# Kernel tuning notes

Measured on AMD Instinct MI355X. Metric: run time of the kernel, lower is better.

The kernel has to match this reference:

```python
import jax, jax.numpy as jnp
import numpy as np

CODEBOOK_NUM = 8192
CODEBOOK_DIM = 256
BETA = 1.0


def setup_inputs() -> dict:
    key = jax.random.key(0)
    k1, k2 = jax.random.split(key)
    z = jax.random.normal(k1, (8, CODEBOOK_DIM, 16, 16, 16), dtype=jnp.float32)
    # torch init: uniform_(-1/codebook_num, 1/codebook_num)
    codebook = jax.random.uniform(
        k2, (CODEBOOK_NUM, CODEBOOK_DIM), dtype=jnp.float32,
        minval=-1.0 / CODEBOOK_NUM, maxval=1.0 / CODEBOOK_NUM)
    return {"z": z, "codebook": codebook}


def reference(z, codebook):
    # z: [B, C, D, H, W] -> [B, D, H, W, C]
    zp = jnp.transpose(z, (0, 2, 3, 4, 1))
    z_flat = zp.reshape(-1, codebook.shape[1])  # [N, C]
    # squared euclidean distances via ||a||^2 + ||b||^2 - 2 a.b
    d = (jnp.sum(z_flat ** 2, axis=1, keepdims=True)
         + jnp.sum(codebook ** 2, axis=1)
         - 2.0 * jnp.matmul(z_flat, codebook.T))  # [N, K]
    idx = jnp.argmin(d, axis=1)  # [N]
    z_q = codebook[idx].reshape(zp.shape)  # [B, D, H, W, C]
    sg = jax.lax.stop_gradient
    loss = jnp.mean((sg(z_q) - zp) ** 2) + BETA * jnp.mean((z_q - sg(zp)) ** 2)
    # straight-through estimator
    z_q_st = zp + sg(z_q - zp)
    out = jnp.transpose(z_q_st, (0, 4, 1, 2, 3))  # back to [B, C, D, H, W]
    return out, loss, idx
```

## Files before the change

### kernel.cpp

```cpp
#include <hip/hip_runtime.h>
#include <hip/hip_bf16.h>
#include <stdint.h>
#include <stddef.h>

typedef unsigned short ushort_t;
typedef unsigned int uint_t;

typedef __attribute__((ext_vector_type(8))) short short8;
typedef __attribute__((ext_vector_type(4))) float floatx4;
typedef __attribute__((ext_vector_type(16))) float floatx16;
typedef __attribute__((ext_vector_type(4))) uint_t uintx4;

#define N_ROWS 32768
#define K_ENT  8192
#define CDIM   256
#define OUT_ELEMS 8388608
#define LOSS_OFF  8388608
#define IDX_OFF   8388609
#define CAP_Q  44
#define MARGIN    2.0e-4f

__device__ __forceinline__ ushort_t f2bf(float f) {
    uint_t x = __float_as_uint(f);
    uint_t r = (x + 0x7fffu + ((x >> 16) & 1u)) >> 16;
    return (ushort_t)r;
}


__device__ __forceinline__ void gload_lds16(const ushort_t* g, ushort_t* s) {
    __builtin_amdgcn_global_load_lds(
        (__attribute__((address_space(1))) void*)(g),
        (__attribute__((address_space(3))) void*)(s), 16, 0, 0);
}

__global__ __launch_bounds__(256) void k_prep(const float* __restrict__ zin,
                                              const float* __restrict__ cb,
                                              ushort_t* __restrict__ zsw,
                                              ushort_t* __restrict__ cbsw,
                                              float* __restrict__ ztf,
                                              int* __restrict__ cnt,
                                              int* __restrict__ cnt2,
                                              double* __restrict__ acc) {
    int bid = blockIdx.x;
    if (bid >= 2048) {
        int t = (bid - 2048) * 256 + threadIdx.x;
        if (t < N_ROWS * 4) cnt[t] = 0;
        if (t == 0) { *acc = 0.0; *cnt2 = 0; }
        int ent = t >> 5;
        int c0  = (t & 31) << 3;
        const float* p = cb + (size_t)ent * CDIM + c0;
        floatx4 f0 = *(const floatx4*)p;
        floatx4 f1 = *(const floatx4*)(p + 4);
        uintx4 pk;
        pk[0] = (uint_t)f2bf(f0[0]) | ((uint_t)f2bf(f0[1]) << 16);
        pk[1] = (uint_t)f2bf(f0[2]) | ((uint_t)f2bf(f0[3]) << 16);
        pk[2] = (uint_t)f2bf(f1[0]) | ((uint_t)f2bf(f1[1]) << 16);
        pk[3] = (uint_t)f2bf(f1[2]) | ((uint_t)f2bf(f1[3]) << 16);
        int idx = (ent >> 5) * 8192 + (c0 >> 4) * 512 + ((c0 >> 3) & 1) * 256 + (ent & 31) * 8;
        *(uintx4*)(cbsw + idx) = pk;
        return;
    }
    __shared__ float lds[64][65];
    int c0 = (bid & 3) << 6;
    int s0 = ((bid >> 2) & 63) << 6;
    int b  = bid >> 8;
    int tid = threadIdx.x;
    int j = tid & 63, ib = tid >> 6;
    const float* zb = zin + ((size_t)b << 20);
#pragma unroll
    for (int rr = 0; rr < 16; ++rr) {
        int i = rr * 4 + ib;
        lds[i][j] = zb[(size_t)(c0 + i) * 4096 + s0 + j];
    }
    __syncthreads();
#pragma unroll
    for (int it = 0; it < 2; ++it) {
        int item = it * 256 + tid;
        int sl = item >> 3;
        int ch = item & 7;
        int row = (b << 12) + s0 + sl;
        int cg  = c0 + ch * 8;
        uintx4 pk;
        floatx4 f0, f1;
#pragma unroll
        for (int q = 0; q < 4; ++q) {
            float a = lds[ch * 8 + 2 * q][sl];
            float bqv = lds[ch * 8 + 2 * q + 1][sl];
            pk[q] = (uint_t)f2bf(a) | ((uint_t)f2bf(bqv) << 16);
        }
#pragma unroll
        for (int q = 0; q < 4; ++q) {
            f0[q] = lds[ch * 8 + q][sl];
            f1[q] = lds[ch * 8 + 4 + q][sl];
        }
        int idx = (row >> 5) * 8192 + (cg >> 4) * 512 + ((cg >> 3) & 1) * 256 + (row & 31) * 8;
        *(uintx4*)(zsw + idx) = pk;
        if (ztf) {
            *(floatx4*)(ztf + (size_t)row * 256 + cg) = f0;
            *(floatx4*)(ztf + (size_t)row * 256 + cg + 4) = f1;
        }
    }
}

__device__ __forceinline__ void screen_emit(const floatx16& acc, float& rmx,
                                            int& cur, int hi, int2* slist,
                                            int ent0) {
    float t0 = fmaxf(fmaxf(acc[0], acc[1]), fmaxf(acc[2], acc[3]));
    float t1 = fmaxf(fmaxf(acc[4], acc[5]), fmaxf(acc[6], acc[7]));
    float t2 = fmaxf(fmaxf(acc[8], acc[9]), fmaxf(acc[10], acc[11]));
    float t3 = fmaxf(fmaxf(acc[12], acc[13]), fmaxf(acc[14], acc[15]));
    float mxo = fmaxf(fmaxf(t0, t1), fmaxf(t2, t3));
    float mx = fmaxf(mxo, __shfl_xor(mxo, 32));
    float rm = fmaxf(rmx, mx);
    rmx = rm;
    float thr = rm - MARGIN;
    if (__any(mxo >= thr)) {
        uint_t mask = 0u;
#pragma unroll
        for (int r = 0; r < 16; ++r)
            if (acc[r] >= thr) mask |= (1u << r);
        int p  = __popc(mask);
        int pp = __shfl_xor(p, 32);
        int s  = cur + (hi ? pp : 0);
        cur += p + pp;
        if (mask) {
#pragma unroll
            for (int r = 0; r < 16; ++r) {
                if (mask & (1u << r)) {
                    if (s < CAP_Q)
                        slist[s] = make_int2(ent0 + (r & 3) + 8 * (r >> 2),
                                             __float_as_int(acc[r]));
                    ++s;
                }
            }
        }
    }
}

__global__ __launch_bounds__(256, 4) void k_screen(const ushort_t* __restrict__ zsw,
                                                   const ushort_t* __restrict__ cbsw,
                                                   int2* __restrict__ surv,
                                                   int* __restrict__ cnt) {
    __shared__ ushort_t bt[2][8192];
    int tid = threadIdx.x;
    int w = tid >> 6, l = tid & 63;
    int bid = blockIdx.x;
    int q  = bid & 3;
    int RB = (bid >> 2) * 128;
    int n = RB + w * 32 + (l & 31);
    int cidx = n * 4 + q;
    int2* slist = surv + (size_t)cidx * CAP_Q;
    int tile0 = q * 64;
    int hi = l & 32;

    auto stage = [&](int t, int b) {
        const ushort_t* gs = cbsw + (size_t)(tile0 + t) * 8192;
#pragma unroll
        for (int j = 0; j < 4; ++j)
            gload_lds16(gs + j * 2048 + tid * 8, &bt[b][j * 2048 + w * 512]);
    };

    stage(0, 0);

    short8 zfr[16];
    {
        const ushort_t* pz = zsw + (size_t)((RB >> 5) + w) * 8192 + l * 8;
#pragma unroll
        for (int s = 0; s < 16; ++s)
            zfr[s] = *(const short8*)(pz + s * 512);
    }
    __syncthreads();

    float rmx = -3.0e38f;
    int cur = 0;
    int esub = (l >> 5) * 4;

    floatx16 accA, accB;
    auto compute = [&](floatx16& acc, int b) {
        const ushort_t* bb = &bt[b][l * 8];
#pragma unroll
        for (int i = 0; i < 16; ++i) acc[i] = 0.f;
#pragma unroll
        for (int s = 0; s < 16; ++s) {
            short8 a = *(const short8*)(bb + s * 512);
            acc = __builtin_amdgcn_mfma_f32_32x32x16_bf16(a, zfr[s], acc, 0, 0, 0);
        }
    };
    auto ent_of = [&](int t) { return (tile0 + t) * 32 + esub; };

    stage(1, 1);
    __builtin_amdgcn_s_setprio(1);
    compute(accA, 0);
    __builtin_amdgcn_s_setprio(0);
    __syncthreads();

    for (int t = 1; t < 63; t += 2) {
        stage(t + 1, (t + 1) & 1);
        __builtin_amdgcn_s_setprio(1);
        compute(accB, t & 1);
        screen_emit(accA, rmx, cur, hi, slist, ent_of(t - 1));
        __builtin_amdgcn_s_setprio(0);
        __syncthreads();
        stage(t + 2, t & 1);
        __builtin_amdgcn_s_setprio(1);
        compute(accA, (t + 1) & 1);
        screen_emit(accB, rmx, cur, hi, slist, ent_of(t));
        __builtin_amdgcn_s_setprio(0);
        __syncthreads();
    }
    __builtin_amdgcn_s_setprio(1);
    compute(accB, 1);
    screen_emit(accA, rmx, cur, hi, slist, ent_of(62));
    __builtin_amdgcn_s_setprio(0);
    screen_emit(accB, rmx, cur, hi, slist, ent_of(63));

    if (!hi) cnt[cidx] = cur;
}

__global__ __launch_bounds__(256) void k_refine(const float* __restrict__ zin,
                                                const float* __restrict__ ztf,
                                                const float* __restrict__ cb,
                                                const int2* __restrict__ surv,
                                                const int* __restrict__ cnt,
                                                int* __restrict__ idxi,
                                                float* __restrict__ idxf) {
    __shared__ float zr[4][256];
    int w = threadIdx.x >> 6, l = threadIdx.x & 63;
    int n = blockIdx.x * 4 + w;
    if (ztf) {
        const float* zrow = ztf + (size_t)n * 256;
#pragma unroll
        for (int i = 0; i < 4; ++i)
            zr[w][l + 64 * i] = zrow[l + 64 * i];
    } else {
        int b = n >> 12, s = n & 4095;
        const float* zb = zin + ((size_t)b << 20) + s;
#pragma unroll
        for (int i = 0; i < 4; ++i)
            zr[w][l + 64 * i] = zb[(size_t)(l + 64 * i) << 12];
    }
    __syncthreads();
    const float* z = zr[w];
    float zn = 0.f;
    for (int c = 0; c < 256; ++c) zn = fmaf(z[c], z[c], zn);

    int c0 = cnt[n * 4 + 0], c1 = cnt[n * 4 + 1];
    int c2 = cnt[n * 4 + 2], c3 = cnt[n * 4 + 3];
    int m = c0 + c1 + c2 + c3;
    bool ok = (c0 <= CAP_Q) && (c1 <= CAP_Q) && (c2 <= CAP_Q) && (c3 <= CAP_Q) && (m >= 1);
    float bu = 3.0e38f;
    int bk = 0x7fffffff;
    if (ok) {
        int myk[3]; float myv[3]; int nc = 0;
        float vmax = -3.0e38f;
        for (int i = l; i < m; i += 64) {
            int qq, s;
            if (i < c0)            { qq = 0; s = i; }
            else if (i < c0 + c1)  { qq = 1; s = i - c0; }
            else if (i < c0 + c1 + c2) { qq = 2; s = i - c0 - c1; }
            else                   { qq = 3; s = i - c0 - c1 - c2; }
            int2 kv = surv[(n * 4 + qq) * CAP_Q + s];
            myk[nc] = kv.x;
            myv[nc] = __int_as_float(kv.y);
            vmax = fmaxf(vmax, myv[nc]);
            ++nc;
        }
#pragma unroll
        for (int msk = 1; msk < 64; msk <<= 1)
            vmax = fmaxf(vmax, __shfl_xor(vmax, msk));
        float fthr = vmax - MARGIN;
        for (int jj = 0; jj < nc; ++jj) {
            if (myv[jj] >= fthr) {
                int k = myk[jj];
                const float* cr = cb + (size_t)k * 256;
                float d = 0.f;
                for (int c = 0; c < 256; c += 4) {
                    floatx4 wv = *(const floatx4*)(cr + c);
                    d = fmaf(z[c], wv[0], d);
                    d = fmaf(z[c + 1], wv[1], d);
                    d = fmaf(z[c + 2], wv[2], d);
                    d = fmaf(z[c + 3], wv[3], d);
                }
                float u = zn - 2.0f * d;
                if (u < bu || (u == bu && k < bk)) { bu = u; bk = k; }
            }
        }
    } else {
        for (int kb = l; kb < K_ENT; kb += 256) {
            const float* p0 = cb + (size_t)(kb)       * 256;
            const float* p1 = cb + (size_t)(kb + 64)  * 256;
            const float* p2 = cb + (size_t)(kb + 128) * 256;
            const float* p3 = cb + (size_t)(kb + 192) * 256;
            float d0 = 0.f, d1 = 0.f, d2 = 0.f, d3 = 0.f;
            for (int c = 0; c < 256; c += 4) {
                floatx4 w0 = *(const floatx4*)(p0 + c);
                floatx4 w1 = *(const floatx4*)(p1 + c);
                floatx4 w2 = *(const floatx4*)(p2 + c);
                floatx4 w3 = *(const floatx4*)(p3 + c);
#pragma unroll
                for (int j = 0; j < 4; ++j) {
                    d0 = fmaf(z[c + j], w0[j], d0);
                    d1 = fmaf(z[c + j], w1[j], d1);
                    d2 = fmaf(z[c + j], w2[j], d2);
                    d3 = fmaf(z[c + j], w3[j], d3);
                }
            }
            float u0 = zn - 2.0f * d0, u1 = zn - 2.0f * d1;
            float u2 = zn - 2.0f * d2, u3 = zn - 2.0f * d3;
            if (u0 < bu) { bu = u0; bk = kb; }
            if (u1 < bu) { bu = u1; bk = kb + 64; }
            if (u2 < bu) { bu = u2; bk = kb + 128; }
            if (u3 < bu) { bu = u3; bk = kb + 192; }
        }
    }
#pragma unroll
    for (int msk = 1; msk < 64; msk <<= 1) {
        float ou = __shfl_xor(bu, msk);
        int   ok2 = __shfl_xor(bk, msk);
        if (ou < bu || (ou == bu && ok2 < bk)) { bu = ou; bk = ok2; }
    }
    if (l == 0) { idxi[n] = bk; idxf[n] = (float)bk; }
}

__global__ __launch_bounds__(256) void k_gather(const float* __restrict__ zin,
                                                const float* __restrict__ cb,
                                                const int* __restrict__ idxi,
                                                float* __restrict__ out,
                                                double* __restrict__ acc,
                                                int* __restrict__ cnt2) {
    __shared__ float tile[64][65];
    __shared__ int lk[64];
    __shared__ float wsum[4];
    int t = threadIdx.x;
    int blk = blockIdx.x;
    int b = blk >> 6;
    int s0 = (blk & 63) << 6;
    int n0 = (b << 12) + s0;
    if (t < 64) lk[t] = idxi[n0 + t];
    __syncthreads();
    int wv = t >> 6, ln = t & 63;
    float ls = 0.f;
#pragma unroll
    for (int ct = 0; ct < 4; ++ct) {
        int c0 = ct << 6;
#pragma unroll
        for (int i = 0; i < 16; ++i) {
            int sl = (wv << 4) + i;
            tile[sl][ln] = cb[(size_t)lk[sl] * 256 + c0 + ln];
        }
        __syncthreads();
        const float* zb = zin + ((size_t)b << 20);
        float* ob = out + ((size_t)b << 20);
#pragma unroll
        for (int j = 0; j < 16; ++j) {
            int cl = (wv << 4) + j;
            size_t o = (size_t)(c0 + cl) * 4096 + s0 + ln;
            float v = tile[ln][cl];
            float zv = zb[o];
            ob[o] = v;
            float d = v - zv;
            ls = fmaf(d, d, ls);
        }
        __syncthreads();
    }
#pragma unroll
    for (int msk = 1; msk < 64; msk <<= 1) ls += __shfl_xor(ls, msk);
    if (ln == 0) wsum[wv] = ls;
    __syncthreads();
    if (t == 0) {
        float tot = (wsum[0] + wsum[1]) + (wsum[2] + wsum[3]);
        atomicAdd(acc, (double)tot);
        __threadfence();
        int done = atomicAdd(cnt2, 1);
        if (done == (int)gridDim.x - 1) {
            __threadfence();
            double v = atomicAdd(acc, 0.0);
            out[LOSS_OFF] = (float)(2.0 * v / 8388608.0);
        }
    }
}

extern "C" void kernel_launch(void* const* d_in, const int* in_sizes, int n_in,
                              void* d_out, int out_size, void* d_ws, size_t ws_size,
                              hipStream_t stream) {
    (void)in_sizes; (void)n_in; (void)out_size;
    const float* z  = (const float*)d_in[0];
    const float* cb = (const float*)d_in[1];
    float* out = (float*)d_out;
    char* ws = (char*)d_ws;

    size_t off = 0;
    ushort_t* zsw  = (ushort_t*)(ws + off); off += 16777216;
    ushort_t* cbsw = (ushort_t*)(ws + off); off += 4194304;
    float* ztf = nullptr;
    const size_t ZTF_BYTES = 33554432;
    const size_t SURV_BYTES = (size_t)N_ROWS * 4 * CAP_Q * 8;
    const size_t TAIL = SURV_BYTES + 524288 + 131072 + 64;
    if (ws_size >= off + ZTF_BYTES + TAIL) { ztf = (float*)(ws + off); off += ZTF_BYTES; }
    int2* surv = (int2*)(ws + off); off += SURV_BYTES;
    int* cnt  = (int*)(ws + off); off += 524288;
    int* idxi = (int*)(ws + off); off += 131072;
    double* acc = (double*)(ws + off); off += 8;
    int* cnt2 = (int*)(ws + off);

    k_prep<<<3072, 256, 0, stream>>>(z, cb, zsw, cbsw, ztf, cnt, cnt2, acc);
    k_screen<<<1024, 256, 0, stream>>>(zsw, cbsw, surv, cnt);
    k_refine<<<8192, 256, 0, stream>>>(z, ztf, cb, surv, cnt, idxi, out + IDX_OFF);
    k_gather<<<8192 / 16, 256, 0, stream>>>(z, cb, idxi, out, acc, cnt2);
}
```

Measured before the change: 359.2 us.

## Compute loss from refine distances and codebook norms, drop z reads in gather

Precomputes codebook squared norms in the prep kernel. The refine kernel then derives each row's squared error as the best distance plus the codeword norm and writes per-block partial losses. The gather kernel no longer reads z or uses atomics; one block reduces the partials in double. The screen kernel's staging pointer arithmetic and accumulator zeroing are also simplified. This saves a full read of z in gather, at the cost of a serialized final reduction in block 0 and an fp32 algebraic loss that may differ slightly from the directly computed one.

```diff
diff --git a/kernel.cpp b/kernel.cpp
--- a/kernel.cpp
+++ b/kernel.cpp
@@ -38,14 +38,10 @@
                                               ushort_t* __restrict__ zsw,
                                               ushort_t* __restrict__ cbsw,
                                               float* __restrict__ ztf,
-                                              int* __restrict__ cnt,
-                                              int* __restrict__ cnt2,
-                                              double* __restrict__ acc) {
+                                              float* __restrict__ cn) {
     int bid = blockIdx.x;
     if (bid >= 2048) {
         int t = (bid - 2048) * 256 + threadIdx.x;
-        if (t < N_ROWS * 4) cnt[t] = 0;
-        if (t == 0) { *acc = 0.0; *cnt2 = 0; }
         int ent = t >> 5;
         int c0  = (t & 31) << 3;
         const float* p = cb + (size_t)ent * CDIM + c0;
@@ -58,6 +54,14 @@
         pk[3] = (uint_t)f2bf(f1[2]) | ((uint_t)f2bf(f1[3]) << 16);
         int idx = (ent >> 5) * 8192 + (c0 >> 4) * 512 + ((c0 >> 3) & 1) * 256 + (ent & 31) * 8;
         *(uintx4*)(cbsw + idx) = pk;
+        float pn = 0.f;
+#pragma unroll
+        for (int qq = 0; qq < 4; ++qq) pn = fmaf(f0[qq], f0[qq], pn);
+#pragma unroll
+        for (int qq = 0; qq < 4; ++qq) pn = fmaf(f1[qq], f1[qq], pn);
+#pragma unroll
+        for (int m = 1; m < 32; m <<= 1) pn += __shfl_xor(pn, m);
+        if ((t & 31) == 0) cn[ent] = pn;
         return;
     }
     __shared__ float lds[64][65];
@@ -153,14 +157,15 @@
     int tile0 = q * 64;
     int hi = l & 32;
 
-    auto stage = [&](int t, int b) {
-        const ushort_t* gs = cbsw + (size_t)(tile0 + t) * 8192;
+    const ushort_t* gsp = cbsw + (size_t)tile0 * 8192 + tid * 8;
+    auto stage = [&](ushort_t* ld) {
 #pragma unroll
         for (int j = 0; j < 4; ++j)
-            gload_lds16(gs + j * 2048 + tid * 8, &bt[b][j * 2048 + w * 512]);
+            gload_lds16(gsp + j * 2048, ld + j * 2048);
+        gsp += 8192;
     };
 
-    stage(0, 0);
+    stage(&bt[0][w * 512]);
 
     short8 zfr[16];
     {
@@ -175,35 +180,39 @@
     int cur = 0;
     int esub = (l >> 5) * 4;
 
+    floatx16 zacc;
+#pragma unroll
+    for (int i = 0; i < 16; ++i) zacc[i] = 0.f;
+
     floatx16 accA, accB;
     auto compute = [&](floatx16& acc, int b) {
         const ushort_t* bb = &bt[b][l * 8];
-#pragma unroll
-        for (int i = 0; i < 16; ++i) acc[i] = 0.f;
-#pragma unroll
-        for (int s = 0; s < 16; ++s) {
+        short8 a0 = *(const short8*)(bb);
+        acc = __builtin_amdgcn_mfma_f32_32x32x16_bf16(a0, zfr[0], zacc, 0, 0, 0);
+#pragma unroll
+        for (int s = 1; s < 16; ++s) {
             short8 a = *(const short8*)(bb + s * 512);
             acc = __builtin_amdgcn_mfma_f32_32x32x16_bf16(a, zfr[s], acc, 0, 0, 0);
         }
     };
     auto ent_of = [&](int t) { return (tile0 + t) * 32 + esub; };
 
-    stage(1, 1);
+    stage(&bt[1][w * 512]);
     __builtin_amdgcn_s_setprio(1);
     compute(accA, 0);
     __builtin_amdgcn_s_setprio(0);
     __syncthreads();
 
     for (int t = 1; t < 63; t += 2) {
-        stage(t + 1, (t + 1) & 1);
+        stage(&bt[0][w * 512]);
         __builtin_amdgcn_s_setprio(1);
-        compute(accB, t & 1);
+        compute(accB, 1);
         screen_emit(accA, rmx, cur, hi, slist, ent_of(t - 1));
         __builtin_amdgcn_s_setprio(0);
         __syncthreads();
-        stage(t + 2, t & 1);
+        stage(&bt[1][w * 512]);
         __builtin_amdgcn_s_setprio(1);
-        compute(accA, (t + 1) & 1);
+        compute(accA, 0);
         screen_emit(accB, rmx, cur, hi, slist, ent_of(t));
         __builtin_amdgcn_s_setprio(0);
         __syncthreads();
@@ -223,8 +232,11 @@
                                                 const int2* __restrict__ surv,
                                                 const int* __restrict__ cnt,
                                                 int* __restrict__ idxi,
-                                                float* __restrict__ idxf) {
+                                                float* __restrict__ idxf,
+                                                const float* __restrict__ cn,
+                                                float* __restrict__ lossp) {
     __shared__ float zr[4][256];
+    __shared__ float lossw[4];
     int w = threadIdx.x >> 6, l = threadIdx.x & 63;
     int n = blockIdx.x * 4 + w;
     if (ztf) {
@@ -319,18 +331,23 @@
         int   ok2 = __shfl_xor(bk, msk);
         if (ou < bu || (ou == bu && ok2 < bk)) { bu = ou; bk = ok2; }
     }
-    if (l == 0) { idxi[n] = bk; idxf[n] = (float)bk; }
-}
-
-__global__ __launch_bounds__(256) void k_gather(const float* __restrict__ zin,
-                                                const float* __restrict__ cb,
+    if (l == 0) {
+        idxi[n] = bk;
+        idxf[n] = (float)bk;
+        lossw[w] = bu + cn[bk];
+    }
+    __syncthreads();
+    if (threadIdx.x == 0)
+        lossp[blockIdx.x] = (lossw[0] + lossw[1]) + (lossw[2] + lossw[3]);
+}
+
+__global__ __launch_bounds__(256) void k_gather(const float* __restrict__ cb,
                                                 const int* __restrict__ idxi,
-                                                float* __restrict__ out,
-                                                double* __restrict__ acc,
-                                                int* __restrict__ cnt2) {
+                                                const float* __restrict__ lossp,
+                                                float* __restrict__ out) {
     __shared__ float tile[64][65];
     __shared__ int lk[64];
-    __shared__ float wsum[4];
+    __shared__ double dsum[4];
     int t = threadIdx.x;
     int blk = blockIdx.x;
     int b = blk >> 6;
@@ -339,7 +356,7 @@
     if (t < 64) lk[t] = idxi[n0 + t];
     __syncthreads();
     int wv = t >> 6, ln = t & 63;
-    float ls = 0.f;
+    float* ob = out + ((size_t)b << 20);
 #pragma unroll
     for (int ct = 0; ct < 4; ++ct) {
         int c0 = ct << 6;
@@ -349,34 +366,23 @@
             tile[sl][ln] = cb[(size_t)lk[sl] * 256 + c0 + ln];
         }
         __syncthreads();
-        const float* zb = zin + ((size_t)b << 20);
-        float* ob = out + ((size_t)b << 20);
 #pragma unroll
         for (int j = 0; j < 16; ++j) {
             int cl = (wv << 4) + j;
-            size_t o = (size_t)(c0 + cl) * 4096 + s0 + ln;
-            float v = tile[ln][cl];
-            float zv = zb[o];
-            ob[o] = v;
-            float d = v - zv;
-            ls = fmaf(d, d, ls);
+            ob[(size_t)(c0 + cl) * 4096 + s0 + ln] = tile[ln][cl];
         }
         __syncthreads();
     }
-#pragma unroll
-    for (int msk = 1; msk < 64; msk <<= 1) ls += __shfl_xor(ls, msk);
-    if (ln == 0) wsum[wv] = ls;
-    __syncthreads();
-    if (t == 0) {
-        float tot = (wsum[0] + wsum[1]) + (wsum[2] + wsum[3]);
-        atomicAdd(acc, (double)tot);
-        __threadfence();
-        int done = atomicAdd(cnt2, 1);
-        if (done == (int)gridDim.x - 1) {
-            __threadfence();
-            double v = atomicAdd(acc, 0.0);
-            out[LOSS_OFF] = (float)(2.0 * v / 8388608.0);
-        }
+    if (blk == 0) {
+        double s = 0.0;
+        for (int i = t; i < 8192; i += 256) s += (double)lossp[i];
+#pragma unroll
+        for (int msk = 1; msk < 64; msk <<= 1) s += __shfl_xor(s, msk);
+        if (ln == 0) dsum[wv] = s;
+        __syncthreads();
+        if (t == 0)
+            out[LOSS_OFF] = (float)(2.0 * ((dsum[0] + dsum[1]) + (dsum[2] + dsum[3]))
+                                    / 8388608.0);
     }
 }
 
@@ -395,16 +401,16 @@
     float* ztf = nullptr;
     const size_t ZTF_BYTES = 33554432;
     const size_t SURV_BYTES = (size_t)N_ROWS * 4 * CAP_Q * 8;
-    const size_t TAIL = SURV_BYTES + 524288 + 131072 + 64;
+    const size_t TAIL = SURV_BYTES + 524288 + 131072 + 32768 + 32768;
     if (ws_size >= off + ZTF_BYTES + TAIL) { ztf = (float*)(ws + off); off += ZTF_BYTES; }
     int2* surv = (int2*)(ws + off); off += SURV_BYTES;
-    int* cnt  = (int*)(ws + off); off += 524288;
-    int* idxi = (int*)(ws + off); off += 131072;
-    double* acc = (double*)(ws + off); off += 8;
-    int* cnt2 = (int*)(ws + off);
-
-    k_prep<<<3072, 256, 0, stream>>>(z, cb, zsw, cbsw, ztf, cnt, cnt2, acc);
+    int* cnt    = (int*)(ws + off); off += 524288;
+    int* idxi   = (int*)(ws + off); off += 131072;
+    float* cn   = (float*)(ws + off); off += 32768;
+    float* lossp = (float*)(ws + off); off += 32768;
+
+    k_prep<<<3072, 256, 0, stream>>>(z, cb, zsw, cbsw, ztf, cn);
     k_screen<<<1024, 256, 0, stream>>>(zsw, cbsw, surv, cnt);
-    k_refine<<<8192, 256, 0, stream>>>(z, ztf, cb, surv, cnt, idxi, out + IDX_OFF);
-    k_gather<<<8192 / 16, 256, 0, stream>>>(z, cb, idxi, out, acc, cnt2);
-}
+    k_refine<<<8192, 256, 0, stream>>>(z, ztf, cb, surv, cnt, idxi, out + IDX_OFF, cn, lossp);
+    k_gather<<<8192 / 16, 256, 0, stream>>>(cb, idxi, lossp, out);
+}
```

Result: faster. 336.2 us (-6.4%).
